# Kernel tuning notes

Measured on AMD Instinct MI355X. Metric: run time of the kernel, lower is better.

Reference implementation:

```python
import jax, jax.numpy as jnp
import numpy as np

HIDDEN = 1024
HEAD = 64
B, T = 4, 4096

def setup_inputs() -> dict:
    key = jax.random.key(0)
    kx, kq, kk, kv = jax.random.split(key, 4)
    bound = 1.0 / np.sqrt(HIDDEN)  # nn.Linear default init range
    x = jax.random.normal(kx, (B, T, HIDDEN), dtype=jnp.float32)
    W_Q = jax.random.uniform(kq, (HIDDEN, HEAD), jnp.float32, -bound, bound)
    W_K = jax.random.uniform(kk, (HIDDEN, HEAD), jnp.float32, -bound, bound)
    W_V = jax.random.uniform(kv, (HIDDEN, HEAD), jnp.float32, -bound, bound)
    return {"x": x, "W_Q": W_Q, "W_K": W_K, "W_V": W_V}

def reference(x, W_Q, W_K, W_V):
    # Q,K,V: [B,T,HEAD]
    Q = x @ W_Q
    K = x @ W_K
    V = x @ W_V
    scale = 1.0 / np.sqrt(HEAD).astype(np.float32)
    scores = jnp.einsum('bqd,bkd->bqk', Q, K) * scale  # [B,T,T]
    Tlen = x.shape[1]
    causal = jnp.tril(jnp.ones((Tlen, Tlen), dtype=bool))
    scores = jnp.where(causal, scores, -jnp.inf)
    attn = jax.nn.softmax(scores, axis=-1)
    # dropout=0.0 -> identity
    return jnp.einsum('bqk,bkd->bqd', attn, V)
```

## Files before the change

### kernel.cpp

```cpp
#include <hip/hip_runtime.h>

typedef short bf16x8 __attribute__((ext_vector_type(8)));
typedef float f32x4 __attribute__((ext_vector_type(4)));

#define T_LEN 4096
#define NB    4
#define HID   1024
#define HD    64

__device__ __forceinline__ unsigned short f2bf(float f) {
    union { float f; unsigned int u; } v; v.f = f;
    unsigned int u = v.u;
    u += 0x7fffu + ((u >> 16) & 1u);
    return (unsigned short)(u >> 16);
}

__device__ __forceinline__ void gl_lds16(const float* g, float* l) {
    __builtin_amdgcn_global_load_lds(
        (const __attribute__((address_space(1))) unsigned int*)g,
        (__attribute__((address_space(3))) unsigned int*)l, 16, 0, 0);
}

__global__ __launch_bounds__(256) void wtrans_kernel(
    const float* __restrict__ wq, const float* __restrict__ wk,
    const float* __restrict__ wv, unsigned short* __restrict__ Wpk)
{
    const int idx = blockIdx.x * 256 + threadIdx.x;
    const int k = idx & 1023;
    const int n = idx >> 10;
    const float* w = (n < 64) ? wq : ((n < 128) ? wk : wv);
    const int ks = k >> 5, g = (k >> 3) & 3, j = k & 7;
    const int nt = n >> 4, lr = n & 15;
    const int lane = g * 16 + lr;
    Wpk[((size_t)(ks * 12 + nt) << 9) + (lane << 3) + j] =
        f2bf(w[(size_t)k * 64 + (n & 63)]);
}

__global__ __launch_bounds__(256, 2) void qkv_proj_kernel(
    const float* __restrict__ x, const unsigned short* __restrict__ Wpk,
    unsigned short* __restrict__ Qb, unsigned short* __restrict__ Kpk,
    unsigned short* __restrict__ Vpk)
{
    __shared__ __align__(16) float xs[2][1024];
    const int tid = threadIdx.x;
    const int w = tid >> 6, lane = tid & 63;
    const int g = lane >> 4, lr = lane & 15;
    const int t0 = blockIdx.x * 32;
    const int mh = w & 1, nh = w >> 1;
    const int arow = mh * 16 + lr;
    const int rx = lr & 7;

    const int srow = (w << 3) + (lane >> 3);
    const int schunk = (lane & 7) ^ (lane >> 3);
    const float* gstage = x + (size_t)(t0 + srow) * HID + (schunk << 2);
    const int ldst = w << 8;

    f32x4 acc[6];
#pragma unroll
    for (int i = 0; i < 6; ++i) acc[i] = (f32x4)(0.0f);

    gl_lds16(gstage, &xs[0][ldst]);
    __syncthreads();

    for (int t = 0; t < 32; ++t) {
        const int cur = t & 1;
        if (t < 31) gl_lds16(gstage + (t + 1) * 32, &xs[cur ^ 1][ldst]);

        const float4 a0 = *(const float4*)&xs[cur][arow * 32 + (((g * 2) ^ rx) << 2)];
        const float4 a1 = *(const float4*)&xs[cur][arow * 32 + (((g * 2 + 1) ^ rx) << 2)];
        bf16x8 af;
        af[0] = (short)f2bf(a0.x); af[1] = (short)f2bf(a0.y);
        af[2] = (short)f2bf(a0.z); af[3] = (short)f2bf(a0.w);
        af[4] = (short)f2bf(a1.x); af[5] = (short)f2bf(a1.y);
        af[6] = (short)f2bf(a1.z); af[7] = (short)f2bf(a1.w);

        const unsigned short* wp = Wpk + (((size_t)(t * 12 + nh * 6)) << 9) + (lane << 3);
#pragma unroll
        for (int j = 0; j < 6; ++j) {
            const bf16x8 bfr = *(const bf16x8*)(wp + ((size_t)j << 9));
            acc[j] = __builtin_amdgcn_mfma_f32_16x16x32_bf16(af, bfr, acc[j], 0, 0, 0);
        }
        __syncthreads();
    }

    const size_t bpk = (size_t)(t0 >> 12) * (T_LEN * HD);
#pragma unroll
    for (int j = 0; j < 6; ++j) {
        const int nt = nh * 6 + j;
#pragma unroll
        for (int r = 0; r < 4; ++r) {
            const int grow = t0 + mh * 16 + g * 4 + r;
            const unsigned short val = f2bf(acc[j][r]);
            if (nt < 4) {
                Qb[(size_t)grow * HD + nt * 16 + lr] = val;
            } else if (nt < 8) {
                const int tl = grow & 4095, d = (nt - 4) * 16 + lr;
                Kpk[bpk + ((((tl >> 4) * 8 + (d >> 3)) * 16 + (tl & 15)) << 3) + (d & 7)] = val;
            } else {
                const int tl = grow & 4095, d = (nt - 8) * 16 + lr;
                Vpk[bpk + (((tl >> 3) * 64 + d) << 3) + (tl & 7)] = val;
            }
        }
    }
}

#define MOFF 96.0f

__device__ __forceinline__ void kv_pair(
    const int t0, const int lane, const int g, const int lr,
    const unsigned short* __restrict__ kpk_b, const unsigned short* __restrict__ vpk_b,
    unsigned short (*P)[136],
    const bf16x8 qf0, const bf16x8 qf1,
    f32x4 oacc[4], float lrow[4])
{
    const float SCL = 0.18033688011112042f;
    f32x4 s[8];
    const unsigned short* kbase = kpk_b + (((size_t)(t0 >> 4)) << 10) + (lane << 3);
#pragma unroll
    for (int nt = 0; nt < 8; ++nt) {
        const bf16x8 kf0 = *(const bf16x8*)(kbase + ((size_t)nt << 10));
        const bf16x8 kf1 = *(const bf16x8*)(kbase + ((size_t)nt << 10) + 512);
        f32x4 a = (f32x4)(0.0f);
        a = __builtin_amdgcn_mfma_f32_16x16x32_bf16(qf0, kf0, a, 0, 0, 0);
        a = __builtin_amdgcn_mfma_f32_16x16x32_bf16(qf1, kf1, a, 0, 0, 0);
        s[nt] = a;
    }
#pragma unroll
    for (int nt = 0; nt < 8; ++nt)
#pragma unroll
        for (int r = 0; r < 4; ++r) {
            const float p = __builtin_amdgcn_exp2f((s[nt][r] - MOFF) * SCL);
            lrow[r] += p;
            P[g * 4 + r][nt * 16 + lr] = f2bf(p);
        }

    const bf16x8 pf0 = *(const bf16x8*)&P[lr][g * 8];
    const bf16x8 pf1 = *(const bf16x8*)&P[lr][32 + g * 8];
    const bf16x8 pf2 = *(const bf16x8*)&P[lr][64 + g * 8];
    const bf16x8 pf3 = *(const bf16x8*)&P[lr][96 + g * 8];
    const unsigned short* vb = vpk_b + (((size_t)((t0 >> 3) + g)) << 9) + (lr << 3);
#pragma unroll
    for (int dt = 0; dt < 4; ++dt) {
        const bf16x8 vf0 = *(const bf16x8*)(vb + dt * 128);
        const bf16x8 vf1 = *(const bf16x8*)(vb + (4 << 9) + dt * 128);
        const bf16x8 vf2 = *(const bf16x8*)(vb + (8 << 9) + dt * 128);
        const bf16x8 vf3 = *(const bf16x8*)(vb + (12 << 9) + dt * 128);
        oacc[dt] = __builtin_amdgcn_mfma_f32_16x16x32_bf16(pf0, vf0, oacc[dt], 0, 0, 0);
        oacc[dt] = __builtin_amdgcn_mfma_f32_16x16x32_bf16(pf1, vf1, oacc[dt], 0, 0, 0);
        oacc[dt] = __builtin_amdgcn_mfma_f32_16x16x32_bf16(pf2, vf2, oacc[dt], 0, 0, 0);
        oacc[dt] = __builtin_amdgcn_mfma_f32_16x16x32_bf16(pf3, vf3, oacc[dt], 0, 0, 0);
    }
}

template <bool MASKED>
__device__ __forceinline__ void kv_single(
    const int t0, const int qw0, const int lane, const int g, const int lr,
    const unsigned short* __restrict__ kpk_b, const unsigned short* __restrict__ vpk_b,
    unsigned short (*P)[136],
    const bf16x8 qf0, const bf16x8 qf1,
    f32x4 oacc[4], float lrow[4])
{
    const float SCL = 0.18033688011112042f;
    f32x4 s[4];
    const unsigned short* kbase = kpk_b + (((size_t)(t0 >> 4)) << 10) + (lane << 3);
#pragma unroll
    for (int nt = 0; nt < 4; ++nt) {
        const bf16x8 kf0 = *(const bf16x8*)(kbase + ((size_t)nt << 10));
        const bf16x8 kf1 = *(const bf16x8*)(kbase + ((size_t)nt << 10) + 512);
        f32x4 a = (f32x4)(0.0f);
        a = __builtin_amdgcn_mfma_f32_16x16x32_bf16(qf0, kf0, a, 0, 0, 0);
        a = __builtin_amdgcn_mfma_f32_16x16x32_bf16(qf1, kf1, a, 0, 0, 0);
        s[nt] = a;
    }
    if (MASKED) {
#pragma unroll
        for (int nt = 0; nt < 4; ++nt) {
            const int kj = t0 + nt * 16 + lr;
#pragma unroll
            for (int r = 0; r < 4; ++r)
                if (kj > qw0 + g * 4 + r) s[nt][r] = -3.0e38f;
        }
    }
#pragma unroll
    for (int nt = 0; nt < 4; ++nt)
#pragma unroll
        for (int r = 0; r < 4; ++r) {
            const float p = __builtin_amdgcn_exp2f((s[nt][r] - MOFF) * SCL);
            lrow[r] += p;
            P[g * 4 + r][nt * 16 + lr] = f2bf(p);
        }

    const bf16x8 pf0 = *(const bf16x8*)&P[lr][g * 8];
    const bf16x8 pf1 = *(const bf16x8*)&P[lr][32 + g * 8];
    const unsigned short* vb = vpk_b + (((size_t)((t0 >> 3) + g)) << 9) + (lr << 3);
#pragma unroll
    for (int dt = 0; dt < 4; ++dt) {
        const bf16x8 vf0 = *(const bf16x8*)(vb + dt * 128);
        const bf16x8 vf1 = *(const bf16x8*)(vb + (4 << 9) + dt * 128);
        oacc[dt] = __builtin_amdgcn_mfma_f32_16x16x32_bf16(pf0, vf0, oacc[dt], 0, 0, 0);
        oacc[dt] = __builtin_amdgcn_mfma_f32_16x16x32_bf16(pf1, vf1, oacc[dt], 0, 0, 0);
    }
}

__global__ __launch_bounds__(64) void attn_part_kernel(
    const unsigned short* __restrict__ Qb, const unsigned short* __restrict__ Kpk,
    const unsigned short* __restrict__ Vpk,
    float* __restrict__ Opart, float* __restrict__ Lpart)
{
    int i = blockIdx.x;
    const int b = i / 1152;
    i -= b * 1152;
    int c = 0, rem = i;
#pragma unroll
    for (int cc = 0; cc < 8; ++cc) {
        const int cnt = 256 - (cc << 5);
        if (c == cc && rem >= cnt) { rem -= cnt; c = cc + 1; }
    }
    const int qt = (c << 5) + rem;

    __shared__ unsigned short Plds[16][136];
    const int lane = threadIdx.x & 63;
    const int g = lane >> 4, lr = lane & 15;
    const int qw0 = qt << 4;
    const int kvbase = c << 9;

    const unsigned short* qp = Qb + (size_t)((b << 12) + qw0 + lr) * HD + g * 8;
    const bf16x8 qf0 = *(const bf16x8*)qp;
    const bf16x8 qf1 = *(const bf16x8*)(qp + 32);
    const unsigned short* kpk_b = Kpk + (size_t)b * (T_LEN * HD);
    const unsigned short* vpk_b = Vpk + (size_t)b * (T_LEN * HD);

    f32x4 oacc[4];
#pragma unroll
    for (int i2 = 0; i2 < 4; ++i2) oacc[i2] = (f32x4)(0.0f);
    float lrow[4] = {0.f, 0.f, 0.f, 0.f};

    const bool diag = ((qt >> 5) == c);
    const int nfull = diag ? ((qw0 - kvbase + 1) >> 6) : 8;
    int it = 0;
    for (; it + 2 <= nfull; it += 2)
        kv_pair(kvbase + it * 64, lane, g, lr, kpk_b, vpk_b, Plds, qf0, qf1, oacc, lrow);
    if (it < nfull)
        kv_single<false>(kvbase + it * 64, qw0, lane, g, lr, kpk_b, vpk_b, Plds,
                         qf0, qf1, oacc, lrow);
    if (diag)
        kv_single<true>(kvbase + nfull * 64, qw0, lane, g, lr, kpk_b, vpk_b, Plds,
                        qf0, qf1, oacc, lrow);

#pragma unroll
    for (int m = 1; m < 16; m <<= 1)
#pragma unroll
        for (int r = 0; r < 4; ++r) lrow[r] += __shfl_xor(lrow[r], m, 64);

    const size_t p = ((size_t)((b << 8) + qt) << 3) + c;
    float* Op = Opart + (p << 10);
    float* Lp = Lpart + (p << 4);
#pragma unroll
    for (int r = 0; r < 4; ++r) {
        const int wrow = g * 4 + r;
        if (lr == 0) Lp[wrow] = lrow[r];
#pragma unroll
        for (int dt = 0; dt < 4; ++dt)
            Op[wrow * 64 + dt * 16 + lr] = oacc[dt][r];
    }
}

__global__ __launch_bounds__(256) void attn_merge_kernel(
    const float* __restrict__ Opart, const float* __restrict__ Lpart,
    float* __restrict__ out)
{
    const int qt = blockIdx.x & 255, b = blockIdx.x >> 8;
    const int nch = (qt >> 5) + 1;
    const int t = threadIdx.x;
    const int row = t >> 4, d0 = (t & 15) << 2;
    const size_t pb = (size_t)blockIdx.x << 3;

    float L = 0.f;
#pragma unroll
    for (int c = 0; c < 8; ++c)
        if (c < nch) L += Lpart[((pb + c) << 4) + row];
    const float inv = 1.0f / L;

    f32x4 o = (f32x4)(0.0f);
#pragma unroll
    for (int c = 0; c < 8; ++c) {
        if (c < nch) {
            const f32x4 v = *(const f32x4*)(Opart + (((pb + c) << 4) + row) * 64 + d0);
#pragma unroll
            for (int j = 0; j < 4; ++j) o[j] += v[j];
        }
    }
    f32x4 res;
#pragma unroll
    for (int j = 0; j < 4; ++j) res[j] = o[j] * inv;
    *(f32x4*)(out + (size_t)((b << 12) + (qt << 4) + row) * HD + d0) = res;
}

extern "C" void kernel_launch(void* const* d_in, const int* in_sizes, int n_in,
                              void* d_out, int out_size, void* d_ws, size_t ws_size,
                              hipStream_t stream) {
    const float* x  = (const float*)d_in[0];
    const float* wq = (const float*)d_in[1];
    const float* wk = (const float*)d_in[2];
    const float* wv = (const float*)d_in[3];
    float* out = (float*)d_out;

    float* Opart = (float*)d_ws;
    float* Lpart = Opart + ((size_t)8192 * 1024);
    unsigned short* Qb  = (unsigned short*)(Lpart + (size_t)8192 * 16);
    unsigned short* Kpk = Qb  + (size_t)NB * T_LEN * HD;
    unsigned short* Vpk = Kpk + (size_t)NB * T_LEN * HD;
    unsigned short* Wpk = Vpk + (size_t)NB * T_LEN * HD;

    wtrans_kernel<<<768, 256, 0, stream>>>(wq, wk, wv, Wpk);
    qkv_proj_kernel<<<512, 256, 0, stream>>>(x, Wpk, Qb, Kpk, Vpk);
    attn_part_kernel<<<NB * 1152, 64, 0, stream>>>(Qb, Kpk, Vpk, Opart, Lpart);
    attn_merge_kernel<<<NB * 256, 256, 0, stream>>>(Opart, Lpart, out);
}
```

Baseline: 75.06 us.

## Shrink QKV projection tile to 16 rows with 128-wide K stages and more blocks

The QKV projection now gives each block 16 token rows instead of 32 and launches twice as many blocks. Each wave owns 3 output column tiles across all 16 rows, instead of 6 tiles over half the rows. The K dimension is staged 128 floats at a time with 4 MFMA steps per barrier, so there are 8 barriers instead of 32. Occupancy is raised to 4 blocks per SIMD to spread the memory-bound x read across more CUs. In exchange, each weight fragment loaded from global memory is reused over fewer rows, so total weight traffic doubles.

```diff
diff --git a/kernel.cpp b/kernel.cpp
--- a/kernel.cpp
+++ b/kernel.cpp
@@ -36,60 +36,67 @@
         f2bf(w[(size_t)k * 64 + (n & 63)]);
 }
 
-__global__ __launch_bounds__(256, 2) void qkv_proj_kernel(
+__global__ __launch_bounds__(256, 4) void qkv_proj_kernel(
     const float* __restrict__ x, const unsigned short* __restrict__ Wpk,
     unsigned short* __restrict__ Qb, unsigned short* __restrict__ Kpk,
     unsigned short* __restrict__ Vpk)
 {
-    __shared__ __align__(16) float xs[2][1024];
+    __shared__ __align__(16) float xs[2][2048];
     const int tid = threadIdx.x;
     const int w = tid >> 6, lane = tid & 63;
     const int g = lane >> 4, lr = lane & 15;
-    const int t0 = blockIdx.x * 32;
-    const int mh = w & 1, nh = w >> 1;
-    const int arow = mh * 16 + lr;
-    const int rx = lr & 7;
-
-    const int srow = (w << 3) + (lane >> 3);
-    const int schunk = (lane & 7) ^ (lane >> 3);
-    const float* gstage = x + (size_t)(t0 + srow) * HID + (schunk << 2);
-    const int ldst = w << 8;
-
-    f32x4 acc[6];
-#pragma unroll
-    for (int i = 0; i < 6; ++i) acc[i] = (f32x4)(0.0f);
-
-    gl_lds16(gstage, &xs[0][ldst]);
+    const int t0 = blockIdx.x * 16;
+
+    const int r0 = (w << 2) + (lane >> 5);
+    const int r1 = r0 + 2;
+    const int pc = lane & 31;
+    const float* gs0 = x + (size_t)(t0 + r0) * HID + ((pc ^ (r0 & 7)) << 2);
+    const float* gs1 = x + (size_t)(t0 + r1) * HID + ((pc ^ (r1 & 7)) << 2);
+    const int lb0 = w << 9;
+    const int lb1 = lb0 + 256;
+
+    f32x4 acc[3];
+#pragma unroll
+    for (int i = 0; i < 3; ++i) acc[i] = (f32x4)(0.0f);
+
+    gl_lds16(gs0, &xs[0][lb0]);
+    gl_lds16(gs1, &xs[0][lb1]);
     __syncthreads();
 
-    for (int t = 0; t < 32; ++t) {
+    for (int t = 0; t < 8; ++t) {
         const int cur = t & 1;
-        if (t < 31) gl_lds16(gstage + (t + 1) * 32, &xs[cur ^ 1][ldst]);
-
-        const float4 a0 = *(const float4*)&xs[cur][arow * 32 + (((g * 2) ^ rx) << 2)];
-        const float4 a1 = *(const float4*)&xs[cur][arow * 32 + (((g * 2 + 1) ^ rx) << 2)];
-        bf16x8 af;
-        af[0] = (short)f2bf(a0.x); af[1] = (short)f2bf(a0.y);
-        af[2] = (short)f2bf(a0.z); af[3] = (short)f2bf(a0.w);
-        af[4] = (short)f2bf(a1.x); af[5] = (short)f2bf(a1.y);
-        af[6] = (short)f2bf(a1.z); af[7] = (short)f2bf(a1.w);
-
-        const unsigned short* wp = Wpk + (((size_t)(t * 12 + nh * 6)) << 9) + (lane << 3);
-#pragma unroll
-        for (int j = 0; j < 6; ++j) {
-            const bf16x8 bfr = *(const bf16x8*)(wp + ((size_t)j << 9));
-            acc[j] = __builtin_amdgcn_mfma_f32_16x16x32_bf16(af, bfr, acc[j], 0, 0, 0);
+        if (t < 7) {
+            gl_lds16(gs0 + (t + 1) * 128, &xs[cur ^ 1][lb0]);
+            gl_lds16(gs1 + (t + 1) * 128, &xs[cur ^ 1][lb1]);
+        }
+#pragma unroll
+        for (int kk = 0; kk < 4; ++kk) {
+            const int lc0 = kk * 8 + g * 2;
+            const float4 a0 = *(const float4*)&xs[cur][lr * 128 + ((lc0 ^ (lr & 7)) << 2)];
+            const float4 a1 = *(const float4*)&xs[cur][lr * 128 + (((lc0 + 1) ^ (lr & 7)) << 2)];
+            bf16x8 af;
+            af[0] = (short)f2bf(a0.x); af[1] = (short)f2bf(a0.y);
+            af[2] = (short)f2bf(a0.z); af[3] = (short)f2bf(a0.w);
+            af[4] = (short)f2bf(a1.x); af[5] = (short)f2bf(a1.y);
+            af[6] = (short)f2bf(a1.z); af[7] = (short)f2bf(a1.w);
+            const unsigned short* wp =
+                Wpk + (((size_t)((t * 4 + kk) * 12 + w * 3)) << 9) + (lane << 3);
+#pragma unroll
+            for (int j = 0; j < 3; ++j) {
+                const bf16x8 bfr = *(const bf16x8*)(wp + ((size_t)j << 9));
+                acc[j] = __builtin_amdgcn_mfma_f32_16x16x32_bf16(af, bfr, acc[j], 0, 0, 0);
+            }
         }
         __syncthreads();
     }
 
     const size_t bpk = (size_t)(t0 >> 12) * (T_LEN * HD);
 #pragma unroll
-    for (int j = 0; j < 6; ++j) {
-        const int nt = nh * 6 + j;
+    for (int j = 0; j < 3; ++j) {
+        const int nt = w * 3 + j;
 #pragma unroll
         for (int r = 0; r < 4; ++r) {
-            const int grow = t0 + mh * 16 + g * 4 + r;
+            const int grow = t0 + g * 4 + r;
             const unsigned short val = f2bf(acc[j][r]);
             if (nt < 4) {
                 Qb[(size_t)grow * HD + nt * 16 + lr] = val;
@@ -313,7 +320,7 @@
     unsigned short* Wpk = Vpk + (size_t)NB * T_LEN * HD;
 
     wtrans_kernel<<<768, 256, 0, stream>>>(wq, wk, wv, Wpk);
-    qkv_proj_kernel<<<512, 256, 0, stream>>>(x, Wpk, Qb, Kpk, Vpk);
+    qkv_proj_kernel<<<1024, 256, 0, stream>>>(x, Wpk, Qb, Kpk, Vpk);
     attn_part_kernel<<<NB * 1152, 64, 0, stream>>>(Qb, Kpk, Vpk, Opart, Lpart);
     attn_merge_kernel<<<NB * 256, 256, 0, stream>>>(Opart, Lpart, out);
 }
```

Result: faster. 66.74 us (-11.1%).
